# Performance work log

Measured on AMD Instinct MI355X. Metric: run time of the kernel, lower is better.

Reference implementation:

```python
import jax, jax.numpy as jnp
import numpy as np

D = 768        # d_model
NH = 12        # n_head
HD = D // NH   # head_dim = 64
T = 8          # num_frames
SCALE = 1.0
LN_EPS = 1e-5


def _layer_norm(x, g, b):
    # fp16-safe LayerNorm: compute in fp32, cast back (matches LayerNorm subclass)
    x32 = x.astype(jnp.float32)
    mu = jnp.mean(x32, axis=-1, keepdims=True)
    var = jnp.mean(jnp.square(x32 - mu), axis=-1, keepdims=True)
    y = (x32 - mu) / jnp.sqrt(var + LN_EPS) * g + b
    return y.astype(x.dtype)


def _adapter(x, w1, b1, w2, b2):
    # Adapter with skip_connect=False: fc1 -> exact GELU -> fc2
    h = jax.nn.gelu(x @ w1.T + b1, approximate=False)
    return h @ w2.T + b2


def _mha(xq, ykv, w_in, b_in, w_out, b_out, need_weights=False):
    # xq: (Tx, N, D), ykv: (Ty, N, D); manual in-proj split like the torch code
    q = xq @ w_in[:D].T + b_in[:D]
    k = ykv @ w_in[D:2 * D].T + b_in[D:2 * D]
    v = ykv @ w_in[2 * D:].T + b_in[2 * D:]
    Tx, N = q.shape[0], q.shape[1]
    Ty = k.shape[0]
    q = q.reshape(Tx, N, NH, HD).transpose(1, 2, 0, 3)  # (N, H, Tx, hd)
    k = k.reshape(Ty, N, NH, HD).transpose(1, 2, 0, 3)
    v = v.reshape(Ty, N, NH, HD).transpose(1, 2, 0, 3)
    aff = jnp.einsum('nhqd,nhkd->nhqk', q, k) / jnp.asarray(HD ** 0.5, q.dtype)
    if need_weights:
        # torch does this under no_grad: sum over heads, exp, sum over (Tx*Ty)
        w = jax.lax.stop_gradient(
            jnp.sum(jnp.exp(jnp.sum(aff, axis=1)).reshape(N, -1), axis=-1))
    p = jax.nn.softmax(aff, axis=-1)
    out = jnp.einsum('nhqk,nhkd->nhqd', p, v)
    out = out.transpose(2, 0, 1, 3).reshape(Tx, N, D)
    out = out @ w_out.T + b_out
    if need_weights:
        return out, w
    return out


def setup_inputs() -> dict:
    key = jax.random.key(0)
    ks = jax.random.split(key, 12)
    DH = D // 4  # adapter hidden = 192

    def w(k, shape):
        return jax.random.normal(k, shape, jnp.float32) * 0.02

    z = lambda *s: jnp.zeros(s, jnp.float32)
    return {
        'x': jax.random.normal(ks[0], (197, 64, D), jnp.float32),
        'in_proj_w': w(ks[1], (3 * D, D)), 'in_proj_b': z(3 * D),
        'out_proj_w': w(ks[2], (D, D)), 'out_proj_b': z(D),
        'ln1_g': jnp.ones((D,), jnp.float32), 'ln1_b': z(D),
        'ln2_g': jnp.ones((D,), jnp.float32), 'ln2_b': z(D),
        'fc_w': w(ks[3], (4 * D, D)), 'fc_b': z(4 * D),
        'proj_w': w(ks[4], (D, 4 * D)), 'proj_b': z(D),
        'sa1_w': w(ks[5], (DH, D)), 'sa1_b': z(DH),
        'sa2_w': w(ks[6], (D, DH)), 'sa2_b': z(D),
        'ta1_w': w(ks[7], (DH, D)), 'ta1_b': z(DH),
        'ta2_w': w(ks[8], (D, DH)), 'ta2_b': z(D),
        'ma1_w': w(ks[9], (DH, D)), 'ma1_b': z(DH),
        'ma2_w': w(ks[10], (D, DH)), 'ma2_b': z(D),
    }


def reference(x, in_proj_w, in_proj_b, out_proj_w, out_proj_b,
              ln1_g, ln1_b, ln2_g, ln2_b, fc_w, fc_b, proj_w, proj_b,
              sa1_w, sa1_b, sa2_w, sa2_b, ta1_w, ta1_b, ta2_w, ta2_b,
              ma1_w, ma1_b, ma2_w, ma2_b):
    n, bt, d = x.shape
    b = bt // T
    # temporal attention on the class token: 'n (b t) d -> t (b n) d'
    ct = x[0]                                   # (bt, d)
    xt = ct.reshape(b, T, d).transpose(1, 0, 2)  # (T, b, d)
    xt = _mha(_layer_norm(xt, ln1_g, ln1_b), _layer_norm(xt, ln1_g, ln1_b),
              in_proj_w, in_proj_b, out_proj_w, out_proj_b)
    xt = _adapter(xt, ta1_w, ta1_b, ta2_w, ta2_b)
    xt = xt.transpose(1, 0, 2).reshape(1, bt, d)  # 't (b n) d -> n (b t) d'

    xln = _layer_norm(x, ln1_g, ln1_b)
    ori_attn, ori_w = _mha(xln, xln, in_proj_w, in_proj_b,
                           out_proj_w, out_proj_b, need_weights=True)
    crs_attn, crs_w = _mha(xln, xt, in_proj_w, in_proj_b,
                           out_proj_w, out_proj_b, need_weights=True)
    lam = (crs_w / (crs_w + ori_w))[None, :, None]  # (1, bt, 1)
    x = x + (1.0 - lam) * ori_attn \
          + SCALE * _adapter(lam * crs_attn, sa1_w, sa1_b, sa2_w, sa2_b)

    xn = _layer_norm(x, ln2_g, ln2_b)
    h = xn @ fc_w.T + fc_b
    h = h * jax.nn.sigmoid(1.702 * h)  # QuickGELU
    mlp_out = h @ proj_w.T + proj_b
    x = x + mlp_out + SCALE * _adapter(xn, ma1_w, ma1_b, ma2_w, ma2_b)
    return x
```

## Files before the change

kernel.cpp:

```cpp
#include <hip/hip_runtime.h>
#include <hip/hip_bf16.h>
#include <math.h>


typedef __attribute__((ext_vector_type(8))) short bf16x8;
typedef __attribute__((ext_vector_type(4))) float f32x4;

__device__ __forceinline__ float bf2f(short s) {
  unsigned u = ((unsigned)(unsigned short)s) << 16;
  float f;
  __builtin_memcpy(&f, &u, 4);
  return f;
}
__device__ __forceinline__ short f2bf(float f) {
  __hip_bfloat16 h = __float2bfloat16(f);
  short s;
  __builtin_memcpy(&s, &h, 2);
  return s;
}

__device__ __forceinline__ void gld16(void* lds, const void* g) {
  __builtin_amdgcn_global_load_lds(
      (const __attribute__((address_space(1))) unsigned int*)g,
      (__attribute__((address_space(3))) unsigned int*)lds, 16, 0, 0);
}

struct WPair { const float* s; short* d; int n; };
struct WArr { WPair p[10]; };

__global__ __launch_bounds__(256)
void convert_k(WArr a) {
  WPair w = a.p[blockIdx.y];
  for (int i = blockIdx.x * 256 + threadIdx.x; i < w.n; i += gridDim.x * 256)
    w.d[i] = f2bf(w.s[i]);
}

__global__ __launch_bounds__(256)
void ln_k(const float* __restrict__ in, const float* __restrict__ g,
          const float* __restrict__ b, short* __restrict__ out) {
  const int t = blockIdx.x;
  const float* xr = in + (size_t)t * 768;
  const int tid = threadIdx.x;
  float v0 = xr[tid], v1 = xr[tid + 256], v2 = xr[tid + 512];
  float s = v0 + v1 + v2;
#pragma unroll
  for (int m = 1; m < 64; m <<= 1) s += __shfl_xor(s, m);
  __shared__ float red[4];
  if ((tid & 63) == 0) red[tid >> 6] = s;
  __syncthreads();
  float mu = (red[0] + red[1] + red[2] + red[3]) * (1.f / 768.f);
  __syncthreads();
  float d0 = v0 - mu, d1 = v1 - mu, d2 = v2 - mu;
  float q = d0 * d0 + d1 * d1 + d2 * d2;
#pragma unroll
  for (int m = 1; m < 64; m <<= 1) q += __shfl_xor(q, m);
  if ((tid & 63) == 0) red[tid >> 6] = q;
  __syncthreads();
  float rstd = rsqrtf((red[0] + red[1] + red[2] + red[3]) * (1.f / 768.f) + 1e-5f);
  size_t o = (size_t)t * 768;
  out[o + tid]       = f2bf(d0 * rstd * g[tid]       + b[tid]);
  out[o + tid + 256] = f2bf(d1 * rstd * g[tid + 256] + b[tid + 256]);
  out[o + tid + 512] = f2bf(d2 * rstd * g[tid + 512] + b[tid + 512]);
}

template <int ACT, int EPI>
__global__ __launch_bounds__(256)
void gemm_k(const short* __restrict__ A, int lda,
            const short* __restrict__ W,
            const float* __restrict__ bias,
            short* __restrict__ outb, float* __restrict__ outf,
            const float* __restrict__ lam,
            int M, int N, int K) {
  __shared__ short As[64][40];
  __shared__ short Ws[64][40];
  const int tid = threadIdx.x;
  const int n0 = blockIdx.x * 64;
  const int m0 = blockIdx.y * 64;
  const int lane = tid & 63, w = tid >> 6;
  const int wr = w >> 1, wc = w & 1;
  const int g = lane >> 4, li = lane & 15;
  const int srow = tid >> 2, scol = (tid & 3) * 8;

  f32x4 acc[2][2];
#pragma unroll
  for (int i = 0; i < 2; i++)
#pragma unroll
    for (int j = 0; j < 2; j++) acc[i][j] = (f32x4){0.f, 0.f, 0.f, 0.f};

  const short* Aptr = A + (size_t)(m0 + srow) * lda + scol;
  const short* Wptr = W + (size_t)(n0 + srow) * K + scol;

  for (int kk = 0; kk < K; kk += 32) {
    __syncthreads();
    *(bf16x8*)&As[srow][scol] = *(const bf16x8*)(Aptr + kk);
    *(bf16x8*)&Ws[srow][scol] = *(const bf16x8*)(Wptr + kk);
    __syncthreads();
    bf16x8 a[2], b[2];
#pragma unroll
    for (int mi = 0; mi < 2; ++mi)
      a[mi] = *(const bf16x8*)&As[wr * 32 + mi * 16 + li][g * 8];
#pragma unroll
    for (int ni = 0; ni < 2; ++ni)
      b[ni] = *(const bf16x8*)&Ws[wc * 32 + ni * 16 + li][g * 8];
#pragma unroll
    for (int mi = 0; mi < 2; ++mi)
#pragma unroll
      for (int ni = 0; ni < 2; ++ni)
        acc[mi][ni] = __builtin_amdgcn_mfma_f32_16x16x32_bf16(
            a[mi], b[ni], acc[mi][ni], 0, 0, 0);
  }

#pragma unroll
  for (int mi = 0; mi < 2; ++mi)
#pragma unroll
    for (int ni = 0; ni < 2; ++ni)
#pragma unroll
      for (int r = 0; r < 4; ++r) {
        int row = m0 + wr * 32 + mi * 16 + g * 4 + r;
        int col = n0 + wc * 32 + ni * 16 + li;
        float v = acc[mi][ni][r];
        if (bias) v += bias[col];
        if (ACT == 1) v = v / (1.f + __expf(-1.702f * v));
        if (ACT == 2) v = 0.5f * v * (1.f + erff(v * 0.70710678118f));
        size_t idx = (size_t)row * N + col;
        if (EPI == 0) outb[idx] = f2bf(v);
        else if (EPI == 1) outf[idx] = v;
        else if (EPI == 5) outb[idx] = f2bf(v * lam[row]);
      }
}

template <int ACT, int EPI>
__global__ __launch_bounds__(512, 6)
void gemm512_k(const short* __restrict__ A, int lda,
               const short* __restrict__ W,
               const float* __restrict__ bias,
               short* __restrict__ outb, float* __restrict__ outf,
               const float* __restrict__ lam,
               const float* __restrict__ addv,
               const float* __restrict__ resid,
               const short* __restrict__ A2, int lda2,
               const short* __restrict__ W2,
               const float* __restrict__ bias2, int K2,
               int M, int N, int K, int nx) {
  int nwg = gridDim.x;
  int orig = blockIdx.x;
  int q = nwg >> 3, r = nwg & 7;
  int xcd = orig & 7, cidx = orig >> 3;
  int wgid = (xcd < r ? xcd * (q + 1) : r * (q + 1) + (xcd - r) * q) + cidx;
  const int n0 = (wgid % nx) * 128;
  const int m0 = (wgid / nx) * 128;

  __shared__ short As[2][128][32];
  __shared__ short Ws[2][128][32];
  const int tid = threadIdx.x;
  const int w = tid >> 6, lane = tid & 63;
  const int g = lane >> 4, li = lane & 15;
  const int wr = w >> 2, wc = w & 3;

  const int srow = tid >> 2;
  const int scol = ((tid & 3) ^ ((tid >> 3) & 3)) * 8;
  const int cxr  = (g ^ ((li >> 1) & 3)) * 8;

  f32x4 acc[4][2];
#pragma unroll
  for (int i = 0; i < 4; i++)
#pragma unroll
    for (int j = 0; j < 2; j++) acc[i][j] = (f32x4){0.f, 0.f, 0.f, 0.f};

  int ar = m0 + srow; if (ar > M - 1) ar = M - 1;
  const short* Ap = A + (size_t)ar * lda + scol;
  const short* Wp = W + (size_t)(n0 + srow) * K + scol;
  const short* A2b = A2 ? A2 : A;
  const short* W2b = W2 ? W2 : W;
  const short* Bp = A2b + (size_t)ar * lda2 + scol;
  const short* Vp = W2b + (size_t)(n0 + srow) * K2 + scol;

  const int ks1 = K >> 5;
  const int ks2 = A2 ? (K2 >> 5) : 0;
  const int total = ks1 + ks2;

  auto STAGE = [&](int s, int bi) {
    if (s < ks1) {
      const int kk = s * 32;
      gld16(&As[bi][w * 16][0], Ap + kk);
      gld16(&Ws[bi][w * 16][0], Wp + kk);
    } else {
      const int kk = (s - ks1) * 32;
      gld16(&As[bi][w * 16][0], Bp + kk);
      gld16(&Ws[bi][w * 16][0], Vp + kk);
    }
  };

  STAGE(0, 0);

  for (int t = 0; t < total; ++t) {
    const int bi = t & 1;
    if (t + 1 < total) {
      STAGE(t + 1, bi ^ 1);
      asm volatile("s_waitcnt vmcnt(2)" ::: "memory");
    } else {
      asm volatile("s_waitcnt vmcnt(0)" ::: "memory");
    }
    __builtin_amdgcn_s_barrier();

    bf16x8 a[4], b[2];
#pragma unroll
    for (int mi = 0; mi < 4; ++mi)
      a[mi] = *(const bf16x8*)&As[bi][wr * 64 + mi * 16 + li][cxr];
#pragma unroll
    for (int ni = 0; ni < 2; ++ni)
      b[ni] = *(const bf16x8*)&Ws[bi][wc * 32 + ni * 16 + li][cxr];
    asm volatile("s_waitcnt lgkmcnt(0)" ::: "memory");
    __builtin_amdgcn_sched_barrier(0);
#pragma unroll
    for (int mi = 0; mi < 4; ++mi)
#pragma unroll
      for (int ni = 0; ni < 2; ++ni)
        acc[mi][ni] = __builtin_amdgcn_mfma_f32_16x16x32_bf16(
            a[mi], b[ni], acc[mi][ni], 0, 0, 0);
    __builtin_amdgcn_s_barrier();
  }

#pragma unroll
  for (int mi = 0; mi < 4; ++mi)
#pragma unroll
    for (int ni = 0; ni < 2; ++ni)
#pragma unroll
      for (int r = 0; r < 4; ++r) {
        int row = m0 + wr * 64 + mi * 16 + g * 4 + r;
        int col = n0 + wc * 32 + ni * 16 + li;
        if (row >= M) continue;
        float v = acc[mi][ni][r];
        if (bias) v += bias[col];
        if (bias2) v += bias2[col];
        if (ACT == 1) v = v / (1.f + __expf(-1.702f * v));
        if (ACT == 2) v = 0.5f * v * (1.f + erff(v * 0.70710678118f));
        size_t idx = (size_t)row * N + col;
        if (EPI == 0) outb[idx] = f2bf(v);
        else if (EPI == 2) {
          float l = lam[row & 63];
          outf[idx] = resid[idx] + (1.f - l) * v + addv[(size_t)(row & 63) * 768 + col];
        } else if (EPI == 6) outf[idx] = resid[idx] + v;
      }
}

__global__ __launch_bounds__(256)
void attn_k(const short* __restrict__ qkv, short* __restrict__ attn_out) {
  const int n = blockIdx.x;
  const int h = blockIdx.y;
  const int tid = threadIdx.x;
  const int lane = tid & 63, w = tid >> 6;
  const int g = lane >> 4, li = lane & 15;

  __shared__ short Vt[64][232];
  __shared__ short Pl[4][16][232];

  {
    const int d = tid & 63;
    for (int key = tid >> 6; key < 224; key += 4) {
      short v = 0;
      if (key < 197)
        v = qkv[(size_t)(key * 64 + n) * 2304 + 1536 + h * 64 + d];
      Vt[d][key] = v;
    }
  }
  __syncthreads();

  const short* Qb = qkv + (size_t)n * 2304 + h * 64;
  const short* Kb = Qb + 768;

  for (int mt = w; mt < 13; mt += 4) {
    const int m0 = mt * 16;
    int arow = m0 + li;
    if (arow > 196) arow = 196;
    bf16x8 a0 = *(const bf16x8*)(Qb + (size_t)arow * 147456 + g * 8);
    bf16x8 a1 = *(const bf16x8*)(Qb + (size_t)arow * 147456 + 32 + g * 8);

    float s[13][4];
#pragma unroll
    for (int nt = 0; nt < 13; ++nt) {
      int kc = nt * 16 + li;
      if (kc > 196) kc = 196;
      bf16x8 b0 = *(const bf16x8*)(Kb + (size_t)kc * 147456 + g * 8);
      bf16x8 b1 = *(const bf16x8*)(Kb + (size_t)kc * 147456 + 32 + g * 8);
      f32x4 acc = (f32x4){0.f, 0.f, 0.f, 0.f};
      acc = __builtin_amdgcn_mfma_f32_16x16x32_bf16(a0, b0, acc, 0, 0, 0);
      acc = __builtin_amdgcn_mfma_f32_16x16x32_bf16(a1, b1, acc, 0, 0, 0);
#pragma unroll
      for (int r = 0; r < 4; ++r) s[nt][r] = acc[r] * 0.125f;
    }

#pragma unroll
    for (int r = 0; r < 4; ++r) {
      float mx = -1e30f;
#pragma unroll
      for (int nt = 0; nt < 13; ++nt) {
        if (nt * 16 + li >= 197) s[nt][r] = -1e30f;
        mx = fmaxf(mx, s[nt][r]);
      }
      mx = fmaxf(mx, __shfl_xor(mx, 1));
      mx = fmaxf(mx, __shfl_xor(mx, 2));
      mx = fmaxf(mx, __shfl_xor(mx, 4));
      mx = fmaxf(mx, __shfl_xor(mx, 8));
      float sum = 0.f;
#pragma unroll
      for (int nt = 0; nt < 13; ++nt) {
        float e = (s[nt][r] <= -1e29f) ? 0.f : __expf(s[nt][r] - mx);
        s[nt][r] = e;
        sum += e;
      }
      sum += __shfl_xor(sum, 1);
      sum += __shfl_xor(sum, 2);
      sum += __shfl_xor(sum, 4);
      sum += __shfl_xor(sum, 8);
      float inv = 1.f / sum;
#pragma unroll
      for (int nt = 0; nt < 13; ++nt) s[nt][r] *= inv;
    }

#pragma unroll
    for (int r = 0; r < 4; ++r) {
      int row = g * 4 + r;
#pragma unroll
      for (int nt = 0; nt < 13; ++nt)
        Pl[w][row][nt * 16 + li] = f2bf(s[nt][r]);
      Pl[w][row][208 + li] = 0;
    }
    asm volatile("s_waitcnt lgkmcnt(0)" ::: "memory");
    __builtin_amdgcn_sched_barrier(0);

    f32x4 o[4];
#pragma unroll
    for (int ni = 0; ni < 4; ++ni) o[ni] = (f32x4){0.f, 0.f, 0.f, 0.f};
#pragma unroll
    for (int kk = 0; kk < 7; ++kk) {
      bf16x8 pa = *(const bf16x8*)&Pl[w][li][kk * 32 + g * 8];
#pragma unroll
      for (int ni = 0; ni < 4; ++ni) {
        bf16x8 vb = *(const bf16x8*)&Vt[ni * 16 + li][kk * 32 + g * 8];
        o[ni] = __builtin_amdgcn_mfma_f32_16x16x32_bf16(pa, vb, o[ni], 0, 0, 0);
      }
    }
#pragma unroll
    for (int ni = 0; ni < 4; ++ni)
#pragma unroll
      for (int r = 0; r < 4; ++r) {
        int prow = m0 + g * 4 + r;
        if (prow < 197)
          attn_out[(size_t)(prow * 64 + n) * 768 + h * 64 + ni * 16 + li] =
              f2bf(o[ni][r]);
      }
  }
}

__global__ __launch_bounds__(256)
void lam_part_k(const short* __restrict__ qkv, float* __restrict__ eo_part) {
  const int n = blockIdx.x;
  const int mt = blockIdx.y;
  const int tid = threadIdx.x;
  const int lane = tid & 63, w = tid >> 6;
  const int g = lane >> 4, li = lane & 15;
  const short* Qb = qkv + (size_t)n * 2304;
  const short* Kb = Qb + 768;

  int arow = mt * 16 + li;
  if (arow > 196) arow = 196;
  const short* Ap = Qb + (size_t)arow * 147456;

  bf16x8 a[24];
#pragma unroll
  for (int s = 0; s < 24; ++s)
    a[s] = *(const bf16x8*)(Ap + s * 32 + g * 8);

  float eo = 0.f;
  for (int nt = w; nt < 13; nt += 4) {
    int kc = nt * 16 + li;
    if (kc > 196) kc = 196;
    const short* Bp = Kb + (size_t)kc * 147456;
    f32x4 acc = (f32x4){0.f, 0.f, 0.f, 0.f};
#pragma unroll
    for (int s = 0; s < 24; ++s) {
      bf16x8 b = *(const bf16x8*)(Bp + s * 32 + g * 8);
      acc = __builtin_amdgcn_mfma_f32_16x16x32_bf16(a[s], b, acc, 0, 0, 0);
    }
#pragma unroll
    for (int r = 0; r < 4; ++r) {
      int prow = mt * 16 + g * 4 + r;
      int col = nt * 16 + li;
      if (prow < 197 && col < 197) eo += __expf(acc[r] * 0.125f);
    }
  }

#pragma unroll
  for (int m = 1; m < 64; m <<= 1) eo += __shfl_xor(eo, m);
  __shared__ float red[4];
  if (lane == 0) red[w] = eo;
  __syncthreads();
  if (tid == 0)
    eo_part[n * 13 + mt] = red[0] + red[1] + red[2] + red[3];
}

__global__ __launch_bounds__(64)
void lam_fin_k(const short* __restrict__ qkv, const short* __restrict__ kvt,
               const float* __restrict__ eo_part, float* __restrict__ lam) {
  const int n = blockIdx.x;
  const int lane = threadIdx.x;
  const short* kt = kvt + (size_t)n * 1536;

  float ec = 0.f;
  for (int p = lane; p < 197; p += 64) {
    const short* qp = qkv + (size_t)n * 2304 + (size_t)p * 147456;
    float dot = 0.f;
    for (int d0 = 0; d0 < 768; d0 += 8) {
      bf16x8 qa = *(const bf16x8*)(qp + d0);
      bf16x8 ka = *(const bf16x8*)(kt + d0);
#pragma unroll
      for (int j = 0; j < 8; ++j) dot += bf2f(qa[j]) * bf2f(ka[j]);
    }
    ec += __expf(dot * 0.125f);
  }
#pragma unroll
  for (int m = 1; m < 64; m <<= 1) ec += __shfl_xor(ec, m);

  if (lane == 0) {
    float eo = 0.f;
#pragma unroll
    for (int t = 0; t < 13; ++t) eo += eo_part[n * 13 + t];
    lam[n] = ec / (ec + eo);
  }
}

__global__ __launch_bounds__(64)
void tattn_k(const short* __restrict__ qkv, short* __restrict__ attn_t) {
  const int bb = blockIdx.x, h = blockIdx.y;
  const int tid = threadIdx.x;
  __shared__ float sm[8][9];
  {
    const int tt = tid >> 3, ss = tid & 7;
    const short* q = qkv + (size_t)(bb * 8 + tt) * 2304 + h * 64;
    const short* k = qkv + (size_t)(bb * 8 + ss) * 2304 + 768 + h * 64;
    float dot = 0.f;
#pragma unroll
    for (int d = 0; d < 64; d += 8) {
      bf16x8 qa = *(const bf16x8*)(q + d);
      bf16x8 ka = *(const bf16x8*)(k + d);
#pragma unroll
      for (int j = 0; j < 8; ++j) dot += bf2f(qa[j]) * bf2f(ka[j]);
    }
    sm[tt][ss] = dot * 0.125f;
  }
  __syncthreads();
  if (tid < 8) {
    float mx = -1e30f;
#pragma unroll
    for (int s2 = 0; s2 < 8; ++s2) mx = fmaxf(mx, sm[tid][s2]);
    float sum = 0.f;
#pragma unroll
    for (int s2 = 0; s2 < 8; ++s2) {
      float e = __expf(sm[tid][s2] - mx);
      sm[tid][s2] = e;
      sum += e;
    }
    float inv = 1.f / sum;
#pragma unroll
    for (int s2 = 0; s2 < 8; ++s2) sm[tid][s2] *= inv;
  }
  __syncthreads();
  {
    const int d = tid;
    float v[8];
#pragma unroll
    for (int s2 = 0; s2 < 8; ++s2)
      v[s2] = bf2f(qkv[(size_t)(bb * 8 + s2) * 2304 + 1536 + h * 64 + d]);
#pragma unroll
    for (int tt = 0; tt < 8; ++tt) {
      float o = 0.f;
#pragma unroll
      for (int s2 = 0; s2 < 8; ++s2) o += sm[tt][s2] * v[s2];
      attn_t[(size_t)(bb * 8 + tt) * 768 + h * 64 + d] = f2bf(o);
    }
  }
}

extern "C" void kernel_launch(void* const* d_in, const int* in_sizes, int n_in,
                              void* d_out, int out_size, void* d_ws,
                              size_t ws_size, hipStream_t stream) {
  (void)in_sizes; (void)n_in; (void)out_size; (void)ws_size;

  const float* x          = (const float*)d_in[0];
  const float* in_proj_w  = (const float*)d_in[1];
  const float* in_proj_b  = (const float*)d_in[2];
  const float* out_proj_w = (const float*)d_in[3];
  const float* out_proj_b = (const float*)d_in[4];
  const float* ln1_g      = (const float*)d_in[5];
  const float* ln1_b      = (const float*)d_in[6];
  const float* ln2_g      = (const float*)d_in[7];
  const float* ln2_b      = (const float*)d_in[8];
  const float* fc_w       = (const float*)d_in[9];
  const float* fc_b       = (const float*)d_in[10];
  const float* proj_w     = (const float*)d_in[11];
  const float* proj_b     = (const float*)d_in[12];
  const float* sa1_w      = (const float*)d_in[13];
  const float* sa1_b      = (const float*)d_in[14];
  const float* sa2_w      = (const float*)d_in[15];
  const float* sa2_b      = (const float*)d_in[16];
  const float* ta1_w      = (const float*)d_in[17];
  const float* ta1_b      = (const float*)d_in[18];
  const float* ta2_w      = (const float*)d_in[19];
  const float* ta2_b      = (const float*)d_in[20];
  const float* ma1_w      = (const float*)d_in[21];
  const float* ma1_b      = (const float*)d_in[22];
  const float* ma2_w      = (const float*)d_in[23];
  const float* ma2_b      = (const float*)d_in[24];

  char* ws = (char*)d_ws;
  short* xln  = (short*)(ws + 0);
  short* qkv  = (short*)(ws + 19365888);
  short* hbuf = (short*)(ws + 0);
  short* attn = (short*)(ws + 77463552);
  short* h2   = (short*)(ws + 77463552);
  float* x1   = (float*)(ws + 96829440);
  short* xn   = (short*)(ws + 135561216);

  char* wreg = ws + 154927104;
  short* w_inproj  = (short*)(wreg + 0);
  short* w_outproj = (short*)(wreg + 3538944);
  short* w_fc      = (short*)(wreg + 4718592);
  short* w_proj    = (short*)(wreg + 9437184);
  short* w_sa1     = (short*)(wreg + 14155776);
  short* w_sa2     = (short*)(wreg + 14450688);
  short* w_ta1     = (short*)(wreg + 14745600);
  short* w_ta2     = (short*)(wreg + 15040512);
  short* w_ma1     = (short*)(wreg + 15335424);
  short* w_ma2     = (short*)(wreg + 15630336);

  char* sm = ws + 170852352;
  short* attn_t  = (short*)(sm + 0);
  short* tproj   = (short*)(sm + 98304);
  short* th      = (short*)(sm + 196608);
  short* xt_out  = (short*)(sm + 221184);
  short* kv_t    = (short*)(sm + 319488);
  short* a_in    = (short*)(sm + 516096);
  short* sa_h    = (short*)(sm + 614400);
  float* sa_out  = (float*)(sm + 638976);
  float* lam     = (float*)(sm + 835584);
  float* eo_part = (float*)(sm + 835840);

  float* out = (float*)d_out;

  WArr arr;
  arr.p[0] = {in_proj_w,  w_inproj,  2304 * 768};
  arr.p[1] = {out_proj_w, w_outproj, 768 * 768};
  arr.p[2] = {fc_w,       w_fc,      3072 * 768};
  arr.p[3] = {proj_w,     w_proj,    768 * 3072};
  arr.p[4] = {sa1_w,      w_sa1,     192 * 768};
  arr.p[5] = {sa2_w,      w_sa2,     768 * 192};
  arr.p[6] = {ta1_w,      w_ta1,     192 * 768};
  arr.p[7] = {ta2_w,      w_ta2,     768 * 192};
  arr.p[8] = {ma1_w,      w_ma1,     192 * 768};
  arr.p[9] = {ma2_w,      w_ma2,     768 * 192};
  convert_k<<<dim3(128, 10), 256, 0, stream>>>(arr);

  ln_k<<<12608, 256, 0, stream>>>(x, ln1_g, ln1_b, xln);

  gemm512_k<0, 0><<<18 * 99, 512, 0, stream>>>(
      xln, 768, w_inproj, in_proj_b, qkv, nullptr, nullptr, nullptr, nullptr,
      nullptr, 0, nullptr, nullptr, 32, 12608, 2304, 768, 18);

  lam_part_k<<<dim3(64, 13), 256, 0, stream>>>(qkv, eo_part);

  tattn_k<<<dim3(8, 12), 64, 0, stream>>>(qkv, attn_t);

  gemm_k<0, 0><<<dim3(12, 1), 256, 0, stream>>>(
      attn_t, 768, w_outproj, out_proj_b, tproj, nullptr, nullptr, 64, 768, 768);
  gemm_k<2, 0><<<dim3(3, 1), 256, 0, stream>>>(
      tproj, 768, w_ta1, ta1_b, th, nullptr, nullptr, 64, 192, 768);
  gemm_k<0, 0><<<dim3(12, 1), 256, 0, stream>>>(
      th, 192, w_ta2, ta2_b, xt_out, nullptr, nullptr, 64, 768, 192);
  gemm_k<0, 0><<<dim3(24, 1), 256, 0, stream>>>(
      xt_out, 768, w_inproj + 768 * 768, in_proj_b + 768, kv_t, nullptr,
      nullptr, 64, 1536, 768);

  attn_k<<<dim3(64, 12), 256, 0, stream>>>(qkv, attn);

  lam_fin_k<<<64, 64, 0, stream>>>(qkv, kv_t, eo_part, lam);

  gemm_k<0, 5><<<dim3(12, 1), 256, 0, stream>>>(
      kv_t + 768, 1536, w_outproj, out_proj_b, a_in, nullptr, lam, 64, 768, 768);
  gemm_k<2, 0><<<dim3(3, 1), 256, 0, stream>>>(
      a_in, 768, w_sa1, sa1_b, sa_h, nullptr, nullptr, 64, 192, 768);
  gemm_k<0, 1><<<dim3(12, 1), 256, 0, stream>>>(
      sa_h, 192, w_sa2, sa2_b, nullptr, sa_out, nullptr, 64, 768, 192);

  gemm512_k<0, 2><<<6 * 99, 512, 0, stream>>>(
      attn, 768, w_outproj, out_proj_b, nullptr, x1, lam, sa_out, x,
      nullptr, 0, nullptr, nullptr, 32, 12608, 768, 768, 6);

  ln_k<<<12608, 256, 0, stream>>>(x1, ln2_g, ln2_b, xn);

  gemm512_k<1, 0><<<24 * 99, 512, 0, stream>>>(
      xn, 768, w_fc, fc_b, hbuf, nullptr, nullptr, nullptr, nullptr,
      nullptr, 0, nullptr, nullptr, 32, 12608, 3072, 768, 24);
  gemm_k<2, 0><<<dim3(3, 197), 256, 0, stream>>>(
      xn, 768, w_ma1, ma1_b, h2, nullptr, nullptr, 12608, 192, 768);

  gemm512_k<0, 6><<<6 * 99, 512, 0, stream>>>(
      hbuf, 3072, w_proj, proj_b, nullptr, out, nullptr, nullptr, x1,
      h2, 192, w_ma2, ma2_b, 192, 12608, 768, 3072, 6);
}
```

Baseline: 649.8 us.

## Add 256x128-tile GEMM kernel for QKV and FC projections

Measured after the change: 1.430 ms. +120.1%, slower.

```diff
diff --git a/kernel.cpp b/kernel.cpp
--- a/kernel.cpp
+++ b/kernel.cpp
@@ -126,6 +126,102 @@
         if (EPI == 0) outb[idx] = f2bf(v);
         else if (EPI == 1) outf[idx] = v;
         else if (EPI == 5) outb[idx] = f2bf(v * lam[row]);
+      }
+}
+
+template <int ACT>
+__global__ __launch_bounds__(512, 6)
+void gemm256x128_k(const short* __restrict__ A, int lda,
+                   const short* __restrict__ W,
+                   const float* __restrict__ bias,
+                   short* __restrict__ outb,
+                   int M, int N, int K, int nx) {
+  int nwg = gridDim.x;
+  int orig = blockIdx.x;
+  int q = nwg >> 3, r = nwg & 7;
+  int xcd = orig & 7, cidx = orig >> 3;
+  int wgid = (xcd < r ? xcd * (q + 1) : r * (q + 1) + (xcd - r) * q) + cidx;
+  const int n0 = (wgid % nx) * 128;
+  const int m0 = (wgid / nx) * 256;
+
+  __shared__ short As[2][256][32];
+  __shared__ short Ws[2][128][32];
+  const int tid = threadIdx.x;
+  const int w = tid >> 6, lane = tid & 63;
+  const int g = lane >> 4, li = lane & 15;
+  const int wr = w >> 1, wc = w & 1;
+
+  const int sgc = ((tid & 3) ^ ((tid >> 3) & 3)) * 8;
+  const int cxr = (g ^ ((li >> 1) & 3)) * 8;
+
+  f32x4 acc[4][4];
+#pragma unroll
+  for (int i = 0; i < 4; i++)
+#pragma unroll
+    for (int j = 0; j < 4; j++) acc[i][j] = (f32x4){0.f, 0.f, 0.f, 0.f};
+
+  int arj[2];
+#pragma unroll
+  for (int j = 0; j < 2; ++j) {
+    int rA = m0 + j * 128 + (tid >> 2);
+    arj[j] = rA > M - 1 ? M - 1 : rA;
+  }
+  const short* Ap0 = A + (size_t)arj[0] * lda + sgc;
+  const short* Ap1 = A + (size_t)arj[1] * lda + sgc;
+  const short* Wp  = W + (size_t)(n0 + (tid >> 2)) * K + sgc;
+
+  const int total = K >> 5;
+
+  auto STAGE = [&](int s, int bi) {
+    const int kk = s * 32;
+    gld16(&As[bi][w * 16][0],       Ap0 + kk);
+    gld16(&As[bi][128 + w * 16][0], Ap1 + kk);
+    gld16(&Ws[bi][w * 16][0],       Wp + kk);
+  };
+
+  STAGE(0, 0);
+
+  for (int t = 0; t < total; ++t) {
+    const int bi = t & 1;
+    if (t + 1 < total) {
+      STAGE(t + 1, bi ^ 1);
+      asm volatile("s_waitcnt vmcnt(3)" ::: "memory");
+    } else {
+      asm volatile("s_waitcnt vmcnt(0)" ::: "memory");
+    }
+    __builtin_amdgcn_s_barrier();
+
+    bf16x8 a[4], b[4];
+#pragma unroll
+    for (int mi = 0; mi < 4; ++mi)
+      a[mi] = *(const bf16x8*)&As[bi][wr * 64 + mi * 16 + li][cxr];
+#pragma unroll
+    for (int ni = 0; ni < 4; ++ni)
+      b[ni] = *(const bf16x8*)&Ws[bi][wc * 64 + ni * 16 + li][cxr];
+    asm volatile("s_waitcnt lgkmcnt(0)" ::: "memory");
+    __builtin_amdgcn_sched_barrier(0);
+#pragma unroll
+    for (int mi = 0; mi < 4; ++mi)
+#pragma unroll
+      for (int ni = 0; ni < 4; ++ni)
+        acc[mi][ni] = __builtin_amdgcn_mfma_f32_16x16x32_bf16(
+            a[mi], b[ni], acc[mi][ni], 0, 0, 0);
+    __builtin_amdgcn_s_barrier();
+  }
+
+#pragma unroll
+  for (int mi = 0; mi < 4; ++mi)
+#pragma unroll
+    for (int ni = 0; ni < 4; ++ni)
+#pragma unroll
+      for (int r = 0; r < 4; ++r) {
+        int row = m0 + wr * 64 + mi * 16 + g * 4 + r;
+        int col = n0 + wc * 64 + ni * 16 + li;
+        if (row >= M) continue;
+        float v = acc[mi][ni][r];
+        if (bias) v += bias[col];
+        if (ACT == 1) v = v / (1.f + __expf(-1.702f * v));
+        outb[(size_t)row * N + col] = f2bf(v);
       }
 }
 
@@ -563,9 +659,8 @@
 
   ln_k<<<12608, 256, 0, stream>>>(x, ln1_g, ln1_b, xln);
 
-  gemm512_k<0, 0><<<18 * 99, 512, 0, stream>>>(
-      xln, 768, w_inproj, in_proj_b, qkv, nullptr, nullptr, nullptr, nullptr,
-      nullptr, 0, nullptr, nullptr, 32, 12608, 2304, 768, 18);
+  gemm256x128_k<0><<<50 * 18, 512, 0, stream>>>(
+      xln, 768, w_inproj, in_proj_b, qkv, 12608, 2304, 768, 18);
 
   lam_part_k<<<dim3(64, 13), 256, 0, stream>>>(qkv, eo_part);
 
@@ -598,9 +693,8 @@
 
   ln_k<<<12608, 256, 0, stream>>>(x1, ln2_g, ln2_b, xn);
 
-  gemm512_k<1, 0><<<24 * 99, 512, 0, stream>>>(
-      xn, 768, w_fc, fc_b, hbuf, nullptr, nullptr, nullptr, nullptr,
-      nullptr, 0, nullptr, nullptr, 32, 12608, 3072, 768, 24);
+  gemm256x128_k<1><<<50 * 24, 512, 0, stream>>>(
+      xn, 768, w_fc, fc_b, hbuf, 12608, 3072, 768, 24);
   gemm_k<2, 0><<<dim3(3, 197), 256, 0, stream>>>(
       xn, 768, w_ma1, ma1_b, h2, nullptr, nullptr, 12608, 192, 768);
 
```
